# Optimization experiments

Hardware: AMD Instinct MI355X
Metric: run time of the kernel (lower is better)

The kernel has to match this reference:

```python
import jax, jax.numpy as jnp
import numpy as np

EPS = 1e-8

def elu_feature_map(x):
    return jax.nn.elu(x) + 1.0

def setup_inputs() -> dict:
    key = jax.random.key(0)
    ks = jax.random.split(key, 5)
    B, S, D = 2, 4096, 1024
    scale = 1.0 / np.sqrt(D).astype(np.float32)
    x = jax.random.normal(ks[0], (B, S, D), dtype=jnp.float32)
    Wq = jax.random.normal(ks[1], (D, D), dtype=jnp.float32) * scale
    Wk = jax.random.normal(ks[2], (D, D), dtype=jnp.float32) * scale
    Wv = jax.random.normal(ks[3], (D, D), dtype=jnp.float32) * scale
    Wo = jax.random.normal(ks[4], (D, D), dtype=jnp.float32) * scale
    return {"x": x, "Wq": Wq, "Wk": Wk, "Wv": Wv, "Wo": Wo}

def reference(x, Wq, Wk, Wv, Wo):
    B, S, D = x.shape
    H = 16
    Dh = D // H
    # projections (nn.Linear with no bias: x @ W.T)
    def proj(W):
        return (x @ W.T).reshape(B, S, H, Dh)
    q = elu_feature_map(proj(Wq))  # [B,S,H,Dh]
    k = elu_feature_map(proj(Wk))
    v = proj(Wv)
    # scan over sequence: carry running kv_sum [B,H,Dh,Dh] and k_sum [B,H,Dh]
    q_t = jnp.moveaxis(q, 1, 0)  # [S,B,H,Dh]
    k_t = jnp.moveaxis(k, 1, 0)
    v_t = jnp.moveaxis(v, 1, 0)

    def step(carry, qkv):
        kv_sum, k_sum = carry
        q_i, k_i, v_i = qkv  # each [B,H,Dh]
        kv_sum = kv_sum + jnp.einsum('bhd,bhe->bhde', k_i, v_i)
        k_sum = k_sum + k_i
        num = jnp.einsum('bhd,bhde->bhe', q_i, kv_sum)
        den = jnp.sum(q_i * k_sum, axis=-1, keepdims=True)
        out_i = num / (den + EPS)
        return (kv_sum, k_sum), out_i

    kv0 = jnp.zeros((B, H, Dh, Dh), dtype=x.dtype)
    ks0 = jnp.zeros((B, H, Dh), dtype=x.dtype)
    _, out = jax.lax.scan(step, (kv0, ks0), (q_t, k_t, v_t))  # out: [S,B,H,Dh]
    out = jnp.moveaxis(out, 0, 1).reshape(B, S, D)
    return out @ Wo.T
```

## Files before the change

kernel.cpp:

```cpp
#include <hip/hip_runtime.h>
#include <math.h>


#define EPSF 1e-8f

typedef unsigned short u16;
typedef unsigned int   u32;
typedef __attribute__((ext_vector_type(8))) short short8v;
typedef __attribute__((ext_vector_type(4))) float f32x4;

__device__ __forceinline__ float elu1(float x){ return x > 0.f ? x + 1.f : __expf(x); }
__device__ __forceinline__ u16 f2bf(float f){
    union{float f; u32 i;} c; c.f = f;
    u32 i = c.i + 0x7FFFu + ((c.i >> 16) & 1u);
    return (u16)(i >> 16);
}
__device__ __forceinline__ float bf2f(u16 v){ union{u32 i; float f;} c; c.i = (u32)v << 16; return c.f; }
__device__ __forceinline__ float bflo(u32 v){ union{u32 i; float f;} c; c.i = v << 16; return c.f; }
__device__ __forceinline__ float bfhi(u32 v){ union{u32 i; float f;} c; c.i = v & 0xffff0000u; return c.f; }
__device__ __forceinline__ void f4a(float4 v, float* a){ a[0]=v.x; a[1]=v.y; a[2]=v.z; a[3]=v.w; }

__device__ __forceinline__ void gload16(const void* g, void* l){
    __builtin_amdgcn_global_load_lds((const __attribute__((address_space(1))) u32*)g,
                                     (__attribute__((address_space(3))) u32*)l, 16, 0, 0);
}

__global__ __launch_bounds__(256) void k_cast5(
    const float* __restrict__ x,  const float* __restrict__ wq,
    const float* __restrict__ wk, const float* __restrict__ wv,
    const float* __restrict__ wo,
    u16* __restrict__ xb, u16* __restrict__ wcat, u16* __restrict__ wob)
{
    size_t i8 = ((size_t)blockIdx.x * 256 + threadIdx.x) * 8;
    const float* s; u16* d; size_t off;
    if      (i8 <  8388608) { s = x;  d = xb;            off = i8; }
    else if (i8 <  9437184) { s = wq; d = wcat;          off = i8 - 8388608; }
    else if (i8 < 10485760) { s = wk; d = wcat + 1048576; off = i8 - 9437184; }
    else if (i8 < 11534336) { s = wv; d = wcat + 2097152; off = i8 - 10485760; }
    else                    { s = wo; d = wob;           off = i8 - 11534336; }
    float4 a = *(const float4*)&s[off];
    float4 b = *(const float4*)&s[off + 4];
    uint4 p;
    p.x = (u32)f2bf(a.x) | ((u32)f2bf(a.y) << 16);
    p.y = (u32)f2bf(a.z) | ((u32)f2bf(a.w) << 16);
    p.z = (u32)f2bf(b.x) | ((u32)f2bf(b.y) << 16);
    p.w = (u32)f2bf(b.z) | ((u32)f2bf(b.w) << 16);
    *(uint4*)&d[off] = p;
}

template<int MODE, int NBY>
__global__ __launch_bounds__(256, 2) void k_gemm7(
    const u16* __restrict__ Ag, const u16* __restrict__ Wg, void* __restrict__ Cv)
{
    __shared__ __align__(16) char dsm[73728];
    const int bid = blockIdx.x;
    const int nid = (bid & 7) * ((32 * NBY) >> 3) + (bid >> 3);
    const int bx  = nid / NBY;
    const int by  = nid % NBY;
    const int m0  = bx * 256;
    const int n0  = by * 128;

    const int tid = threadIdx.x;
    const int l   = tid & 63;
    const int wid = tid >> 6;
    const int wm  = wid >> 1;
    const int wn  = wid & 1;
    const int li  = l & 15;
    const int kgi = l >> 4;

    const int ra0 = wm*128 + li;
    const int offA0 = (ra0 >> 1)*128 + (((((ra0 & 1) << 2) | kgi) ^ ((ra0 >> 1) & 7)) << 4);
    const int rb0 = wn*64 + li;
    const int offB0 = (rb0 >> 1)*128 + (((((rb0 & 1) << 2) | kgi) ^ ((rb0 >> 1) & 7)) << 4);

    const int sx   = (l & 7) ^ (l >> 3);
    const int rowb = 2*(wid*8 + (l >> 3)) + (sx >> 2);
    const int skg  = (sx & 3) * 8;
    const u16* srcA = Ag + (size_t)(m0 + rowb) * 1024 + skg;
    const u16* srcB = Wg + (size_t)(n0 + rowb) * 1024 + skg;

    f32x4 acc[8][4];
    #pragma unroll
    for (int m = 0; m < 8; ++m)
        #pragma unroll
        for (int n = 0; n < 4; ++n) acc[m][n] = (f32x4){0.f, 0.f, 0.f, 0.f};

    #define ST7(BUF, T) { \
        char* ab = dsm + (BUF)*24576; \
        char* bb = ab + 16384; \
        _Pragma("unroll") for (int j = 0; j < 4; ++j) \
            gload16(srcA + (size_t)j*65536 + (T)*32, ab + j*4096 + wid*1024); \
        _Pragma("unroll") for (int j = 0; j < 2; ++j) \
            gload16(srcB + (size_t)j*65536 + (T)*32, bb + j*4096 + wid*1024); }

    #define CP7(BUF) { \
        const char* Ab = dsm + (BUF)*24576; \
        const char* Bb = Ab + 16384; \
        short8v bfr[4]; \
        _Pragma("unroll") for (int n = 0; n < 4; ++n) bfr[n] = *(const short8v*)(Bb + offB0 + n*1024); \
        __builtin_amdgcn_s_setprio(1); \
        _Pragma("unroll") for (int m = 0; m < 8; ++m) { \
            short8v afr = *(const short8v*)(Ab + offA0 + m*1024); \
            _Pragma("unroll") for (int n = 0; n < 4; ++n) \
                acc[m][n] = __builtin_amdgcn_mfma_f32_16x16x32_bf16(afr, bfr[n], acc[m][n], 0, 0, 0); \
        } \
        __builtin_amdgcn_s_setprio(0); }

    #define STEP7(CUR, STB, TS) { \
        ST7(STB, TS); \
        CP7(CUR); \
        asm volatile("s_waitcnt vmcnt(6)" ::: "memory"); \
        __builtin_amdgcn_s_barrier(); }

    ST7(0, 0); ST7(1, 1);
    asm volatile("s_waitcnt vmcnt(6)" ::: "memory");
    __builtin_amdgcn_s_barrier();

    #pragma unroll 1
    for (int g = 0; g < 10; ++g) {
        const int t = g * 3;
        STEP7(0, 2, t + 2);
        STEP7(1, 0, t + 3);
        STEP7(2, 1, t + 4);
    }
    CP7(0);
    asm volatile("s_waitcnt vmcnt(0)" ::: "memory");
    __builtin_amdgcn_s_barrier();
    CP7(1);
    #undef STEP7
    #undef CP7
    #undef ST7

    const int r0 = m0 + wm*128 + kgi*4;
    if (MODE == 1) {
        const int matrix = by >> 3;
        const bool do_elu = matrix < 2;
        u16* outp = (u16*)Cv + (size_t)matrix * 8388608;
        const int c0 = (by & 7)*128 + wn*64 + li;
        #pragma unroll
        for (int m = 0; m < 8; ++m)
            #pragma unroll
            for (int n = 0; n < 4; ++n)
                #pragma unroll
                for (int r = 0; r < 4; ++r) {
                    float v = acc[m][n][r];
                    if (do_elu) v = elu1(v);
                    outp[(size_t)(r0 + m*16 + r) * 1024 + c0 + n*16] = f2bf(v);
                }
    } else {
        float* outp = (float*)Cv;
        const int c0 = by*128 + wn*64 + li;
        #pragma unroll
        for (int m = 0; m < 8; ++m)
            #pragma unroll
            for (int n = 0; n < 4; ++n)
                #pragma unroll
                for (int r = 0; r < 4; ++r)
                    outp[(size_t)(r0 + m*16 + r) * 1024 + c0 + n*16] = acc[m][n][r];
    }
}

__global__ __launch_bounds__(256) void k_chunksums(
    const u16* __restrict__ Kg, const u16* __restrict__ Vg,
    u16* __restrict__ CKVb, float* __restrict__ CKS)
{
    const int tid = threadIdx.x;
    const int tx = tid & 15, ty = tid >> 4;
    const int c  = blockIdx.x & 63;
    const int bh = blockIdx.x >> 6;
    const int b = bh >> 4, h = bh & 15;
    const int row0 = b * 4096 + c * 64;
    const int col  = h * 64;

    __shared__ float Ks[64][68];
    __shared__ float Vs[64][68];

    #pragma unroll
    for (int r = 0; r < 2; ++r) {
        int idx = tid + r * 256;
        int i = idx >> 3, cg = (idx & 7) << 3;
        uint4 ku = *(const uint4*)&Kg[(size_t)(row0 + i) * 1024 + col + cg];
        uint4 vu = *(const uint4*)&Vg[(size_t)(row0 + i) * 1024 + col + cg];
        Ks[i][cg+0]=bflo(ku.x); Ks[i][cg+1]=bfhi(ku.x);
        Ks[i][cg+2]=bflo(ku.y); Ks[i][cg+3]=bfhi(ku.y);
        Ks[i][cg+4]=bflo(ku.z); Ks[i][cg+5]=bfhi(ku.z);
        Ks[i][cg+6]=bflo(ku.w); Ks[i][cg+7]=bfhi(ku.w);
        Vs[i][cg+0]=bflo(vu.x); Vs[i][cg+1]=bfhi(vu.x);
        Vs[i][cg+2]=bflo(vu.y); Vs[i][cg+3]=bfhi(vu.y);
        Vs[i][cg+4]=bflo(vu.z); Vs[i][cg+5]=bfhi(vu.z);
        Vs[i][cg+6]=bflo(vu.w); Vs[i][cg+7]=bfhi(vu.w);
    }
    __syncthreads();

    float acc[4][4] = {};
    #pragma unroll 8
    for (int i = 0; i < 64; ++i) {
        float kv[4], vv[4];
        f4a(*(const float4*)&Ks[i][ty*4], kv);
        f4a(*(const float4*)&Vs[i][tx*4], vv);
        #pragma unroll
        for (int a = 0; a < 4; ++a)
            #pragma unroll
            for (int e = 0; e < 4; ++e)
                acc[a][e] = fmaf(kv[a], vv[e], acc[a][e]);
    }
    u16* ckv = &CKVb[(size_t)blockIdx.x * 4096];
    #pragma unroll
    for (int e = 0; e < 4; ++e) {
        u32 p0 = (u32)f2bf(acc[0][e]) | ((u32)f2bf(acc[1][e]) << 16);
        u32 p1 = (u32)f2bf(acc[2][e]) | ((u32)f2bf(acc[3][e]) << 16);
        *(uint2*)&ckv[(tx*4 + e) * 64 + ty*4] = make_uint2(p0, p1);
    }

    if (tid < 64) {
        float s = 0.f;
        #pragma unroll 8
        for (int i = 0; i < 64; ++i) s += Ks[i][tid];
        CKS[(size_t)blockIdx.x * 64 + tid] = s;
    }
}

__global__ __launch_bounds__(256) void k_prefix(u16* __restrict__ CKV, float* __restrict__ CKS)
{
    if (blockIdx.x < 512) {
        const int bh = blockIdx.x >> 4;
        const int p  = ((blockIdx.x & 15) << 8) + threadIdx.x;
        const size_t base = (size_t)bh * 64 * 4096 + p;
        float acc = 0.f;
        #pragma unroll
        for (int c = 0; c < 64; ++c) {
            float t = bf2f(CKV[base + (size_t)c * 4096]);
            CKV[base + (size_t)c * 4096] = f2bf(acc);
            acc += t;
        }
    } else {
        const int idx = (blockIdx.x - 512) * 256 + threadIdx.x;
        const int bh = idx >> 6, d = idx & 63;
        const size_t base = (size_t)bh * 64 * 64 + d;
        float v[64];
        #pragma unroll
        for (int c = 0; c < 64; ++c) v[c] = CKS[base + (size_t)c * 64];
        float acc = 0.f;
        #pragma unroll
        for (int c = 0; c < 64; ++c) { float t = v[c]; CKS[base + (size_t)c * 64] = acc; acc += t; }
    }
}

#define LSTR 72
__global__ __launch_bounds__(256) void k_attn2(
    const u16* __restrict__ Qg, const u16* __restrict__ Kg, const u16* __restrict__ Vg,
    const u16* __restrict__ Stg, const float* __restrict__ KSg, u16* __restrict__ AO)
{
    const int tid = threadIdx.x;
    const int l = tid & 63;
    const int w = tid >> 6;
    const int c  = blockIdx.x & 63;
    const int bh = blockIdx.x >> 6;
    const int row0 = (bh >> 4) * 4096 + c * 64;
    const int col  = (bh & 15) * 64;

    __shared__ __align__(16) u16 Qs [64 * LSTR];
    __shared__ __align__(16) u16 Ks [64 * LSTR];
    __shared__ __align__(16) u16 Vt [64 * LSTR];
    __shared__ __align__(16) u16 Sts[64 * LSTR];
    __shared__ __align__(16) u16 Pl [64 * LSTR];
    __shared__ float ksumF[64];
    __shared__ float invdenL[64];

    #pragma unroll
    for (int r = 0; r < 2; ++r) {
        int idx = tid + r * 256;
        int i = idx >> 3, cg = (idx & 7) << 3;
        *(uint4*)&Qs [i*LSTR + cg] = *(const uint4*)&Qg [(size_t)(row0 + i) * 1024 + col + cg];
        *(uint4*)&Ks [i*LSTR + cg] = *(const uint4*)&Kg [(size_t)(row0 + i) * 1024 + col + cg];
        *(uint4*)&Sts[i*LSTR + cg] = *(const uint4*)&Stg[(size_t)blockIdx.x * 4096 + i * 64 + cg];
        uint4 vu = *(const uint4*)&Vg[(size_t)(row0 + i) * 1024 + col + cg];
        Vt[(cg+0)*LSTR + i] = (u16)(vu.x & 0xffff);
        Vt[(cg+1)*LSTR + i] = (u16)(vu.x >> 16);
        Vt[(cg+2)*LSTR + i] = (u16)(vu.y & 0xffff);
        Vt[(cg+3)*LSTR + i] = (u16)(vu.y >> 16);
        Vt[(cg+4)*LSTR + i] = (u16)(vu.z & 0xffff);
        Vt[(cg+5)*LSTR + i] = (u16)(vu.z >> 16);
        Vt[(cg+6)*LSTR + i] = (u16)(vu.w & 0xffff);
        Vt[(cg+7)*LSTR + i] = (u16)(vu.w >> 16);
    }
    if (tid < 64) ksumF[tid] = KSg[(size_t)blockIdx.x * 64 + tid];
    __syncthreads();

    const int li = l & 15;
    const int lg = l >> 4;
    const int i_row = w * 16 + li;

    short8v bq[2];
    #pragma unroll
    for (int kc = 0; kc < 2; ++kc)
        bq[kc] = *(const short8v*)&Qs[i_row * LSTR + lg*8 + kc*32];

    float den = EPSF;
    #pragma unroll
    for (int mj = 0; mj < 4; ++mj) {
        f32x4 sacc = (f32x4){0.f, 0.f, 0.f, 0.f};
        #pragma unroll
        for (int kc = 0; kc < 2; ++kc) {
            short8v ak = *(const short8v*)&Ks[(mj*16 + li) * LSTR + lg*8 + kc*32];
            sacc = __builtin_amdgcn_mfma_f32_16x16x32_bf16(ak, bq[kc], sacc, 0, 0, 0);
        }
        const int jbase = mj*16 + lg*4;
        float pv[4];
        #pragma unroll
        for (int r = 0; r < 4; ++r) {
            float v = sacc[r];
            v = (jbase + r <= i_row) ? v : 0.f;
            den += v;
            pv[r] = v;
        }
        u32 lo = (u32)f2bf(pv[0]) | ((u32)f2bf(pv[1]) << 16);
        u32 hi = (u32)f2bf(pv[2]) | ((u32)f2bf(pv[3]) << 16);
        *(uint2*)&Pl[i_row * LSTR + jbase] = make_uint2(lo, hi);
    }

    {
        const int d0 = lg * 16;
        uint4 q1 = *(const uint4*)&Qs[i_row * LSTR + d0];
        uint4 q2 = *(const uint4*)&Qs[i_row * LSTR + d0 + 8];
        den += bflo(q1.x)*ksumF[d0+0] + bfhi(q1.x)*ksumF[d0+1]
             + bflo(q1.y)*ksumF[d0+2] + bfhi(q1.y)*ksumF[d0+3]
             + bflo(q1.z)*ksumF[d0+4] + bfhi(q1.z)*ksumF[d0+5]
             + bflo(q1.w)*ksumF[d0+6] + bfhi(q1.w)*ksumF[d0+7]
             + bflo(q2.x)*ksumF[d0+8] + bfhi(q2.x)*ksumF[d0+9]
             + bflo(q2.y)*ksumF[d0+10]+ bfhi(q2.y)*ksumF[d0+11]
             + bflo(q2.z)*ksumF[d0+12]+ bfhi(q2.z)*ksumF[d0+13]
             + bflo(q2.w)*ksumF[d0+14]+ bfhi(q2.w)*ksumF[d0+15];
    }
    den += __shfl_xor(den, 16);
    den += __shfl_xor(den, 32);
    if (l < 16) invdenL[w*16 + l] = 1.f / den;

    f32x4 oacc[4];
    #pragma unroll
    for (int ne = 0; ne < 4; ++ne) oacc[ne] = (f32x4){0.f, 0.f, 0.f, 0.f};
    #pragma unroll
    for (int kc = 0; kc < 2; ++kc) {
        short8v ap = *(const short8v*)&Pl[i_row * LSTR + lg*8 + kc*32];
        short8v aq = bq[kc];
        #pragma unroll
        for (int ne = 0; ne < 4; ++ne) {
            short8v bv = *(const short8v*)&Vt [(ne*16 + li) * LSTR + lg*8 + kc*32];
            short8v bs = *(const short8v*)&Sts[(ne*16 + li) * LSTR + lg*8 + kc*32];
            oacc[ne] = __builtin_amdgcn_mfma_f32_16x16x32_bf16(ap, bv, oacc[ne], 0, 0, 0);
            oacc[ne] = __builtin_amdgcn_mfma_f32_16x16x32_bf16(aq, bs, oacc[ne], 0, 0, 0);
        }
    }

    float inv[4];
    #pragma unroll
    for (int r = 0; r < 4; ++r) inv[r] = invdenL[w*16 + lg*4 + r];
    #pragma unroll
    for (int ne = 0; ne < 4; ++ne)
        #pragma unroll
        for (int r = 0; r < 4; ++r)
            Pl[(w*16 + lg*4 + r) * LSTR + ne*16 + li] = f2bf(oacc[ne][r] * inv[r]);

    #pragma unroll
    for (int p = 0; p < 2; ++p) {
        int idx2 = l + p * 64;
        int ro = w*16 + (idx2 >> 3), cg = (idx2 & 7) << 3;
        *(uint4*)&AO[(size_t)(row0 + ro) * 1024 + col + cg] = *(const uint4*)&Pl[ro*LSTR + cg];
    }
}

extern "C" void kernel_launch(void* const* d_in, const int* in_sizes, int n_in,
                              void* d_out, int out_size, void* d_ws, size_t ws_size,
                              hipStream_t stream)
{
    const float* x  = (const float*)d_in[0];
    const float* Wq = (const float*)d_in[1];
    const float* Wk = (const float*)d_in[2];
    const float* Wv = (const float*)d_in[3];
    const float* Wo = (const float*)d_in[4];
    float* out = (float*)d_out;

    char* w = (char*)d_ws;
    u16*   QKVb = (u16*)(w);
    u16*   Qb   = QKVb;
    u16*   Kb   = QKVb + 8388608;
    u16*   Vb   = QKVb + 16777216;
    u16*   xb   = (u16*)(w + 50331648);
    u16*   AOb  = xb;
    u16*   Wcat = (u16*)(w + 67108864);
    u16*   Wob  = (u16*)(w + 73400320);
    u16*   CKVb = (u16*)(w + 75497472);
    float* CKS  = (float*)(w + 92274688);

    k_cast5       <<<6144, 256, 0, stream>>>(x, Wq, Wk, Wv, Wo, xb, Wcat, Wob);
    k_gemm7<1,24> <<<768,  256, 0, stream>>>(xb, Wcat, (void*)QKVb);
    k_chunksums   <<<2048, 256, 0, stream>>>(Kb, Vb, CKVb, CKS);
    k_prefix      <<<520,  256, 0, stream>>>(CKVb, CKS);
    k_attn2       <<<2048, 256, 0, stream>>>(Qb, Kb, Vb, CKVb, CKS, AOb);
    k_gemm7<3,8>  <<<256,  256, 0, stream>>>(AOb, Wob, (void*)out);
}
```

Measured before the change: 140.4 us.

## Replace QKV projection GEMM with 256x256-tile 8-wave double-buffered kernel

Adds a new QKV projection GEMM that uses 256x256 output tiles, 512 threads (8 waves), 128KB of dynamic LDS with two A/B stage buffers, and a phase-split MFMA schedule using barriers and s_setprio. This doubles the N-tile and so reduces how often A is re-read and how many blocks are launched (384 instead of 768). The goal is higher arithmetic intensity and better overlap of loads with MFMA work. In exchange it uses more LDS and registers per block, which can limit occupancy, and the tightly hand-scheduled vmcnt waits are delicate to get right. The old GEMM is now specialised to the fp32 output projection only.

```diff
diff --git a/kernel.cpp b/kernel.cpp
--- a/kernel.cpp
+++ b/kernel.cpp
@@ -48,9 +48,129 @@
     *(uint4*)&d[off] = p;
 }
 
-template<int MODE, int NBY>
+#define R_A0 0
+#define R_B0 32768
+#define R_A1 65536
+#define R_B1 98304
+
+#define STG8(REG, SRC, T, KH) { \
+    gload16((SRC) + (size_t)(T)*64 + (KH)*32,          dsm + (REG) + (KH)*16384 + wid*1024); \
+    gload16((SRC) + 131072 + (size_t)(T)*64 + (KH)*32, dsm + (REG) + (KH)*16384 + 8192 + wid*1024); }
+
+#define PHA8(REGA, REGB, KK, STCODE) { \
+    _Pragma("unroll") for (int n = 0; n < 4; ++n) \
+        bfr[n] = *(const short8v*)(dsm + (REGB) + (KK)*16384 + offB0 + n*1024); \
+    _Pragma("unroll") for (int m = 0; m < 4; ++m) \
+        afr[m] = *(const short8v*)(dsm + (REGA) + (KK)*16384 + offA0 + m*1024); \
+    STCODE; \
+    asm volatile("s_barrier" ::: "memory"); \
+    __builtin_amdgcn_s_setprio(1); \
+    _Pragma("unroll") for (int m = 0; m < 4; ++m) \
+        _Pragma("unroll") for (int n = 0; n < 4; ++n) \
+            acc[m][n] = __builtin_amdgcn_mfma_f32_16x16x32_bf16(afr[m], bfr[n], acc[m][n], 0, 0, 0); \
+    __builtin_amdgcn_s_setprio(0); \
+    asm volatile("s_barrier" ::: "memory"); }
+
+#define PHB8(REGA, KK, STCODE, WCODE) { \
+    _Pragma("unroll") for (int m = 0; m < 4; ++m) \
+        afr[m] = *(const short8v*)(dsm + (REGA) + (KK)*16384 + 4096 + offA0 + m*1024); \
+    STCODE; \
+    asm volatile("s_barrier" ::: "memory"); \
+    __builtin_amdgcn_s_setprio(1); \
+    _Pragma("unroll") for (int m = 0; m < 4; ++m) \
+        _Pragma("unroll") for (int n = 0; n < 4; ++n) \
+            acc[4+m][n] = __builtin_amdgcn_mfma_f32_16x16x32_bf16(afr[m], bfr[n], acc[4+m][n], 0, 0, 0); \
+    __builtin_amdgcn_s_setprio(0); \
+    WCODE; \
+    asm volatile("s_barrier" ::: "memory"); }
+
+__global__ __launch_bounds__(512, 2) void k_gemm8(
+    const u16* __restrict__ Ag, const u16* __restrict__ Wg, u16* __restrict__ C)
+{
+    extern __shared__ char dsm[];
+    const int bid = blockIdx.x;
+    const int nid = (bid & 7) * 48 + (bid >> 3);
+    const int bx  = nid / 12;
+    const int by  = nid % 12;
+    const int m0  = bx * 256;
+    const int n0  = by * 256;
+
+    const int tid = threadIdx.x;
+    const int l   = tid & 63;
+    const int wid = tid >> 6;
+    const int wm  = wid >> 2;
+    const int wn  = wid & 3;
+    const int li  = l & 15;
+    const int kgi = l >> 4;
+
+    const int ra0 = wm*128 + li;
+    const int offA0 = ((ra0 >> 1) << 7) + (((((ra0 & 1) << 2) | kgi) ^ ((ra0 >> 1) & 7)) << 4);
+    const int rb0 = wn*64 + li;
+    const int offB0 = ((rb0 >> 1) << 7) + (((((rb0 & 1) << 2) | kgi) ^ ((rb0 >> 1) & 7)) << 4);
+
+    const int sx   = (l & 7) ^ (l >> 3);
+    const int rowb = 2*(wid*8 + (l >> 3)) + (sx >> 2);
+    const int skg  = (sx & 3) * 8;
+    const u16* srcA = Ag + (size_t)(m0 + rowb) * 1024 + skg;
+    const u16* srcB = Wg + (size_t)(n0 + rowb) * 1024 + skg;
+
+    f32x4 acc[8][4];
+    #pragma unroll
+    for (int m = 0; m < 8; ++m)
+        #pragma unroll
+        for (int n = 0; n < 4; ++n) acc[m][n] = (f32x4){0.f, 0.f, 0.f, 0.f};
+
+    short8v afr[4], bfr[4];
+
+    STG8(R_A0, srcA, 0, 0); STG8(R_B0, srcB, 0, 0);
+    STG8(R_A0, srcA, 0, 1); STG8(R_B0, srcB, 0, 1);
+    STG8(R_A1, srcA, 1, 0); STG8(R_B1, srcB, 1, 0);
+    asm volatile("s_waitcnt vmcnt(4)" ::: "memory");
+    asm volatile("s_barrier" ::: "memory");
+
+    #pragma unroll 1
+    for (int j = 0; j < 7; ++j) {
+        const int t = 2*j;
+        PHA8(R_A0, R_B0, 0, { STG8(R_A1, srcA, t+1, 1) });
+        PHB8(R_A0, 0,      { STG8(R_B1, srcB, t+1, 1) }, {});
+        PHA8(R_A0, R_B0, 1, { STG8(R_A0, srcA, t+2, 0) });
+        PHB8(R_A0, 1,      { STG8(R_B0, srcB, t+2, 0) },
+             { asm volatile("s_waitcnt vmcnt(4)" ::: "memory"); });
+        PHA8(R_A1, R_B1, 0, { STG8(R_A0, srcA, t+2, 1) });
+        PHB8(R_A1, 0,      { STG8(R_B0, srcB, t+2, 1) }, {});
+        PHA8(R_A1, R_B1, 1, { STG8(R_A1, srcA, t+3, 0) });
+        PHB8(R_A1, 1,      { STG8(R_B1, srcB, t+3, 0) },
+             { asm volatile("s_waitcnt vmcnt(4)" ::: "memory"); });
+    }
+    PHA8(R_A0, R_B0, 0, { STG8(R_A1, srcA, 15, 1) });
+    PHB8(R_A0, 0,      { STG8(R_B1, srcB, 15, 1) }, {});
+    PHA8(R_A0, R_B0, 1, {});
+    PHB8(R_A0, 1, {},  { asm volatile("s_waitcnt vmcnt(0)" ::: "memory"); });
+    PHA8(R_A1, R_B1, 0, {});
+    PHB8(R_A1, 0, {}, {});
+    PHA8(R_A1, R_B1, 1, {});
+    PHB8(R_A1, 1, {}, {});
+
+    const int matrix = by >> 2;
+    const bool do_elu = matrix < 2;
+    u16* outp = C + (size_t)matrix * 8388608;
+    const int r0 = m0 + wm*128 + kgi*4;
+    const int c0 = (by & 3)*256 + wn*64 + li;
+    #pragma unroll
+    for (int m = 0; m < 8; ++m)
+        #pragma unroll
+        for (int n = 0; n < 4; ++n)
+            #pragma unroll
+            for (int r = 0; r < 4; ++r) {
+                float v = acc[m][n][r];
+                if (do_elu) v = elu1(v);
+                outp[(size_t)(r0 + m*16 + r) * 1024 + c0 + n*16] = f2bf(v);
+            }
+}
+
+template<int NBY>
 __global__ __launch_bounds__(256, 2) void k_gemm7(
-    const u16* __restrict__ Ag, const u16* __restrict__ Wg, void* __restrict__ Cv)
+    const u16* __restrict__ Ag, const u16* __restrict__ Wg, float* __restrict__ Cv)
 {
     __shared__ __align__(16) char dsm[73728];
     const int bid = blockIdx.x;
@@ -132,32 +252,14 @@
     #undef ST7
 
     const int r0 = m0 + wm*128 + kgi*4;
-    if (MODE == 1) {
-        const int matrix = by >> 3;
-        const bool do_elu = matrix < 2;
-        u16* outp = (u16*)Cv + (size_t)matrix * 8388608;
-        const int c0 = (by & 7)*128 + wn*64 + li;
-        #pragma unroll
-        for (int m = 0; m < 8; ++m)
+    const int c0 = by*128 + wn*64 + li;
+    #pragma unroll
+    for (int m = 0; m < 8; ++m)
+        #pragma unroll
+        for (int n = 0; n < 4; ++n)
             #pragma unroll
-            for (int n = 0; n < 4; ++n)
-                #pragma unroll
-                for (int r = 0; r < 4; ++r) {
-                    float v = acc[m][n][r];
-                    if (do_elu) v = elu1(v);
-                    outp[(size_t)(r0 + m*16 + r) * 1024 + c0 + n*16] = f2bf(v);
-                }
-    } else {
-        float* outp = (float*)Cv;
-        const int c0 = by*128 + wn*64 + li;
-        #pragma unroll
-        for (int m = 0; m < 8; ++m)
-            #pragma unroll
-            for (int n = 0; n < 4; ++n)
-                #pragma unroll
-                for (int r = 0; r < 4; ++r)
-                    outp[(size_t)(r0 + m*16 + r) * 1024 + c0 + n*16] = acc[m][n][r];
-    }
+            for (int r = 0; r < 4; ++r)
+                Cv[(size_t)(r0 + m*16 + r) * 1024 + c0 + n*16] = acc[m][n][r];
 }
 
 __global__ __launch_bounds__(256) void k_chunksums(
@@ -392,10 +494,13 @@
     u16*   CKVb = (u16*)(w + 75497472);
     float* CKS  = (float*)(w + 92274688);
 
-    k_cast5       <<<6144, 256, 0, stream>>>(x, Wq, Wk, Wv, Wo, xb, Wcat, Wob);
-    k_gemm7<1,24> <<<768,  256, 0, stream>>>(xb, Wcat, (void*)QKVb);
-    k_chunksums   <<<2048, 256, 0, stream>>>(Kb, Vb, CKVb, CKS);
-    k_prefix      <<<520,  256, 0, stream>>>(CKVb, CKS);
-    k_attn2       <<<2048, 256, 0, stream>>>(Qb, Kb, Vb, CKVb, CKS, AOb);
-    k_gemm7<3,8>  <<<256,  256, 0, stream>>>(AOb, Wob, (void*)out);
-}
+    (void)hipFuncSetAttribute(reinterpret_cast<const void*>(k_gemm8),
+                              hipFuncAttributeMaxDynamicSharedMemorySize, 131072);
+
+    k_cast5    <<<6144, 256, 0, stream>>>(x, Wq, Wk, Wv, Wo, xb, Wcat, Wob);
+    k_gemm8    <<<384,  512, 131072, stream>>>(xb, Wcat, QKVb);
+    k_chunksums<<<2048, 256, 0, stream>>>(Kb, Vb, CKVb, CKS);
+    k_prefix   <<<520,  256, 0, stream>>>(CKVb, CKS);
+    k_attn2    <<<2048, 256, 0, stream>>>(Qb, Kb, Vb, CKVb, CKS, AOb);
+    k_gemm7<8> <<<256,  256, 0, stream>>>(AOb, Wob, out);
+}
```

Measured after the change: 144.9 us. 3.2% more time.
